# Kernel optimization log

Measured on AMD Instinct MI355X. Metric: run time of the kernel, lower is better.

Reference implementation:

```python
import jax, jax.numpy as jnp
import numpy as np

BATCH, IN_DIM, UNITS = 2048, 512, 512


def setup_inputs() -> dict:
    key = jax.random.key(0)
    k1, k2 = jax.random.split(key)
    x = jax.random.normal(k1, (BATCH, IN_DIM), dtype=jnp.float32)
    # He-style init for W, shape (1, in_dim, units) as in build()
    W = jax.random.normal(k2, (1, IN_DIM, UNITS), dtype=jnp.float32) * np.float32(np.sqrt(2.0 / IN_DIM))
    bias = jnp.zeros((UNITS,), dtype=jnp.float32)
    return {"x": x, "W": W, "bias": bias}


def reference(x, W, bias):
    # nodal 'exponential': exp(x * w) - 1, broadcast (batch,in,1)*(1,in,units)
    z = jnp.exp(x[:, :, None] * W) - 1.0          # (batch, in, units)
    # pool 'maximum': reduce over input dim
    p = jnp.max(z, axis=1)                         # (batch, units)
    # bias add + activation 'tanh'
    return jnp.tanh(p + bias)
```

## Files before the change

kernel.cpp:

```cpp
#include <hip/hip_runtime.h>


#define BATCH 2048
#define INDIM 512
#define UNITS 512

#define KC 32
#define RB 8
#define NW 16

typedef float v2f __attribute__((ext_vector_type(2)));

__global__ __launch_bounds__(1024, 8) void maxexp_kernel(
    const float* __restrict__ x,
    const float* __restrict__ W,
    const float* __restrict__ bias,
    float* __restrict__ out)
{
    __shared__ float xs[RB][INDIM];
    __shared__ float part[RB][NW][64];

    const int f    = blockIdx.x;
    const int band = (f & 7) * 32 + ((f >> 3) & 31);
    const int ut   = f >> 8;

    const int tid  = threadIdx.x;
    const int lane = tid & 63;
    const int wv   = __builtin_amdgcn_readfirstlane(tid >> 6);
    const int u    = ut * 64 + lane;
    const int k0   = wv * KC;
    const int b0   = band * RB;

    {
        const float4 v = *reinterpret_cast<const float4*>(
            x + (size_t)b0 * INDIM + (size_t)tid * 4);
        *reinterpret_cast<float4*>(&xs[0][0] + (size_t)tid * 4) = v;
    }

    v2f wp[KC / 2];
    {
        const float* wb = W + (size_t)k0 * UNITS + u;
#pragma unroll
        for (int j = 0; j < KC / 2; ++j) {
            v2f t;
            t.x = wb[(size_t)(2 * j)     * UNITS];
            t.y = wb[(size_t)(2 * j + 1) * UNITS];
            wp[j] = t;
        }
    }
#pragma unroll
    for (int j = 0; j < KC / 2; ++j) asm("" : "+v"(wp[j]));

    __syncthreads();

#pragma unroll
    for (int t = 0; t < RB; ++t) {
        const float4* xq = reinterpret_cast<const float4*>(&xs[t][k0]);
        float m0 = -3.4e38f, m1 = -3.4e38f;
#pragma unroll
        for (int q4 = 0; q4 < KC / 4; ++q4) {
            const float4 q = xq[q4];
            v2f a0, a1, p0, p1;
            a0.x = q.x; a0.y = q.y;
            a1.x = q.z; a1.y = q.w;
            asm("v_pk_mul_f32 %0, %1, %2" : "=v"(p0) : "v"(a0), "v"(wp[2 * q4]));
            asm("v_pk_mul_f32 %0, %1, %2" : "=v"(p1) : "v"(a1), "v"(wp[2 * q4 + 1]));
            m0 = fmaxf(fmaxf(m0, p0.x), p0.y);
            m1 = fmaxf(fmaxf(m1, p1.x), p1.y);
        }
        part[t][wv][lane] = fmaxf(m0, m1);
    }

    __syncthreads();

    if (wv < RB) {
        const int t = wv;
        float m = -3.4e38f;
#pragma unroll
        for (int j = 0; j < NW; j += 2)
            m = fmaxf(fmaxf(m, part[t][j][lane]), part[t][j + 1][lane]);
        const float pp = __expf(m) - 1.0f + bias[u];
        const float e  = __expf(2.0f * pp);
        out[(size_t)(b0 + t) * UNITS + u] = 1.0f - 2.0f / (e + 1.0f);
    }
}

extern "C" void kernel_launch(void* const* d_in, const int* in_sizes, int n_in,
                              void* d_out, int out_size, void* d_ws, size_t ws_size,
                              hipStream_t stream) {
    const float* x    = (const float*)d_in[0];
    const float* W    = (const float*)d_in[1];
    const float* bias = (const float*)d_in[2];
    float* out = (float*)d_out;

    dim3 grid(BATCH / RB * (UNITS / 64));
    dim3 block(1024);
    maxexp_kernel<<<grid, block, 0, stream>>>(x, W, bias, out);
}
```

Before: 29.00 us.

## Loop each block over multiple batch bands with double-buffered async x staging

Each block now keeps a 64-row slice of W in registers and iterates over four 8-row batch bands, instead of processing a single band. The next band's x rows are fetched directly into shared memory via global_load_lds into a second buffer while the current band is computed. The point is to amortise W register loads across more work and hide x load latency. In exchange the grid shrinks to 512 blocks of 512 threads, so occupancy and parallelism drop, and there are extra barriers per band.

New measurement: 28.79 us. Within noise of the previous version (-0.7%).

```diff
diff --git a/kernel.cpp b/kernel.cpp
--- a/kernel.cpp
+++ b/kernel.cpp
@@ -5,37 +5,34 @@
 #define INDIM 512
 #define UNITS 512
 
-#define KC 32
+#define KC 64
 #define RB 8
-#define NW 16
+#define NW 8
+#define NBANDS 4
 
 typedef float v2f __attribute__((ext_vector_type(2)));
 
-__global__ __launch_bounds__(1024, 8) void maxexp_kernel(
+__global__ __launch_bounds__(512, 4) void maxexp_kernel(
     const float* __restrict__ x,
     const float* __restrict__ W,
     const float* __restrict__ bias,
     float* __restrict__ out)
 {
-    __shared__ float xs[RB][INDIM];
+    __shared__ float xs[2][RB][INDIM];
     __shared__ float part[RB][NW][64];
 
-    const int f    = blockIdx.x;
-    const int band = (f & 7) * 32 + ((f >> 3) & 31);
-    const int ut   = f >> 8;
+    const int f     = blockIdx.x;
+    const int xcd   = f & 7;
+    const int g     = f >> 3;
+    const int ut    = g & 7;
+    const int bgrp  = g >> 3;
+    const int band0 = xcd * 32 + bgrp * NBANDS;
 
     const int tid  = threadIdx.x;
     const int lane = tid & 63;
     const int wv   = __builtin_amdgcn_readfirstlane(tid >> 6);
     const int u    = ut * 64 + lane;
     const int k0   = wv * KC;
-    const int b0   = band * RB;
-
-    {
-        const float4 v = *reinterpret_cast<const float4*>(
-            x + (size_t)b0 * INDIM + (size_t)tid * 4);
-        *reinterpret_cast<float4*>(&xs[0][0] + (size_t)tid * 4) = v;
-    }
 
     v2f wp[KC / 2];
     {
@@ -51,38 +48,63 @@
 #pragma unroll
     for (int j = 0; j < KC / 2; ++j) asm("" : "+v"(wp[j]));
 
+    const float bv = bias[u];
+
+#define STAGE(buf, bd)                                                        \
+    {                                                                         \
+        const float* src_ = x + (size_t)((bd) * RB + wv) * INDIM + lane * 4;  \
+        float* dst_ = &xs[buf][wv][0];                                        \
+        __builtin_amdgcn_global_load_lds(                                     \
+            (const __attribute__((address_space(1))) unsigned int*)src_,      \
+            (__attribute__((address_space(3))) unsigned int*)dst_, 16, 0, 0); \
+        __builtin_amdgcn_global_load_lds(                                     \
+            (const __attribute__((address_space(1))) unsigned int*)(src_ + 256), \
+            (__attribute__((address_space(3))) unsigned int*)(dst_ + 256), 16, 0, 0); \
+    }
+
+    STAGE(0, band0);
     __syncthreads();
 
+#pragma unroll 1
+    for (int t = 0; t < NBANDS; ++t) {
+        const int band = band0 + t;
+        const int cur  = t & 1;
+
+        if (t + 1 < NBANDS) STAGE(cur ^ 1, band + 1);
+
 #pragma unroll
-    for (int t = 0; t < RB; ++t) {
-        const float4* xq = reinterpret_cast<const float4*>(&xs[t][k0]);
-        float m0 = -3.4e38f, m1 = -3.4e38f;
+        for (int r = 0; r < RB; ++r) {
+            const float4* xq = reinterpret_cast<const float4*>(&xs[cur][r][k0]);
+            float m0 = -3.4e38f, m1 = -3.4e38f;
 #pragma unroll
-        for (int q4 = 0; q4 < KC / 4; ++q4) {
-            const float4 q = xq[q4];
-            v2f a0, a1, p0, p1;
-            a0.x = q.x; a0.y = q.y;
-            a1.x = q.z; a1.y = q.w;
-            asm("v_pk_mul_f32 %0, %1, %2" : "=v"(p0) : "v"(a0), "v"(wp[2 * q4]));
-            asm("v_pk_mul_f32 %0, %1, %2" : "=v"(p1) : "v"(a1), "v"(wp[2 * q4 + 1]));
-            m0 = fmaxf(fmaxf(m0, p0.x), p0.y);
-            m1 = fmaxf(fmaxf(m1, p1.x), p1.y);
+            for (int q = 0; q < KC / 4; ++q) {
+                const float4 a = xq[q];
+                v2f a0, a1, p0, p1;
+                a0.x = a.x; a0.y = a.y;
+                a1.x = a.z; a1.y = a.w;
+                asm("v_pk_mul_f32 %0, %1, %2" : "=v"(p0) : "v"(a0), "v"(wp[2 * q]));
+                asm("v_pk_mul_f32 %0, %1, %2" : "=v"(p1) : "v"(a1), "v"(wp[2 * q + 1]));
+                m0 = fmaxf(fmaxf(m0, p0.x), p0.y);
+                m1 = fmaxf(fmaxf(m1, p1.x), p1.y);
+            }
+            part[r][wv][lane] = fmaxf(m0, m1);
         }
-        part[t][wv][lane] = fmaxf(m0, m1);
+
+        __syncthreads();
+
+        {
+            float m = -3.4e38f;
+#pragma unroll
+            for (int j = 0; j < NW; j += 2)
+                m = fmaxf(fmaxf(m, part[wv][j][lane]), part[wv][j + 1][lane]);
+            const float pp = __expf(m) - 1.0f + bv;
+            const float e  = __expf(2.0f * pp);
+            out[(size_t)(band * RB + wv) * UNITS + u] = 1.0f - 2.0f / (e + 1.0f);
+        }
+
+        __syncthreads();
     }
-
-    __syncthreads();
-
-    if (wv < RB) {
-        const int t = wv;
-        float m = -3.4e38f;
-#pragma unroll
-        for (int j = 0; j < NW; j += 2)
-            m = fmaxf(fmaxf(m, part[t][j][lane]), part[t][j + 1][lane]);
-        const float pp = __expf(m) - 1.0f + bias[u];
-        const float e  = __expf(2.0f * pp);
-        out[(size_t)(b0 + t) * UNITS + u] = 1.0f - 2.0f / (e + 1.0f);
-    }
+#undef STAGE
 }
 
 extern "C" void kernel_launch(void* const* d_in, const int* in_sizes, int n_in,
@@ -93,7 +115,7 @@
     const float* bias = (const float*)d_in[2];
     float* out = (float*)d_out;
 
-    dim3 grid(BATCH / RB * (UNITS / 64));
-    dim3 block(1024);
+    dim3 grid(512);
+    dim3 block(512);
     maxexp_kernel<<<grid, block, 0, stream>>>(x, W, bias, out);
 }
```
